# Kernel optimization log

Hardware: AMD Instinct MI355X
Metric: run time of the kernel (lower is better)

The kernel has to match this reference:

```python
import jax, jax.numpy as jnp
import numpy as np
import itertools

DIM = 384
KEY_DIM = 32
NUM_HEADS = 8
ATTN_RATIO = 4
RESOLUTION = 7
D = ATTN_RATIO * KEY_DIM          # 128
DH = D * NUM_HEADS                # 1024
H_QKV = DH + 2 * KEY_DIM * NUM_HEADS  # 1536
B = 2048
N = RESOLUTION ** 2               # 49


def _build_bias_idxs():
    points = list(itertools.product(range(RESOLUTION), range(RESOLUTION)))
    attention_offsets = {}
    idxs = []
    for p1 in points:
        for p2 in points:
            offset = (abs(p1[0] - p2[0]), abs(p1[1] - p2[1]))
            if offset not in attention_offsets:
                attention_offsets[offset] = len(attention_offsets)
            idxs.append(attention_offsets[offset])
    return np.array(idxs, dtype=np.int32).reshape(N, N), len(attention_offsets)


def setup_inputs() -> dict:
    key = jax.random.key(0)
    ks = jax.random.split(key, 6)
    bias_idxs_np, n_offsets = _build_bias_idxs()  # n_offsets == 49 for resolution 7
    x = jax.random.normal(ks[0], (B, N, DIM), dtype=jnp.float32)
    qkv_w = jax.random.normal(ks[1], (H_QKV, DIM), dtype=jnp.float32) * (DIM ** -0.5)
    qkv_b = jnp.zeros((H_QKV,), dtype=jnp.float32)
    proj_w = jax.random.normal(ks[2], (DIM, DH), dtype=jnp.float32) * (DH ** -0.5)
    proj_b = jnp.zeros((DIM,), dtype=jnp.float32)
    attn_bias = jax.random.normal(ks[3], (NUM_HEADS, n_offsets), dtype=jnp.float32) * 0.02
    bias_idxs = jnp.asarray(bias_idxs_np)
    return {"x": x, "qkv_w": qkv_w, "qkv_b": qkv_b, "proj_w": proj_w,
            "proj_b": proj_b, "attn_bias": attn_bias, "bias_idxs": bias_idxs}


def reference(x, qkv_w, qkv_b, proj_w, proj_b, attn_bias, bias_idxs):
    Bb, Nn, _ = x.shape
    scale = KEY_DIM ** -0.5
    qkv = x @ qkv_w.T + qkv_b                       # [B, N, 1536]
    qkv = qkv.reshape(Bb, Nn, NUM_HEADS, KEY_DIM + KEY_DIM + D)
    q = qkv[..., :KEY_DIM]                          # [B, N, H, kd]
    k = qkv[..., KEY_DIM:2 * KEY_DIM]               # [B, N, H, kd]
    v = qkv[..., 2 * KEY_DIM:]                      # [B, N, H, d]
    bias = attn_bias[:, bias_idxs]                  # [H, N, N] gathered rel-pos bias
    attn = jnp.einsum('bnhk,bmhk->bhnm', q, k) * scale + bias
    attn = jax.nn.softmax(attn, axis=-1)
    out = jnp.einsum('bhnm,bmhd->bnhd', attn, v).reshape(Bb, Nn, DH)
    return out @ proj_w.T + proj_b                  # [B, N, dim]
```

## Files before the change

kernel.cpp:

```cpp
#include <hip/hip_runtime.h>
#include <cstddef>
#include <cstdint>

#define TOK    49
#define KD     32
#define NH     8
#define DHEAD  128
#define HQKV   1536
#define DHTOT  1024
#define DIMM   384

typedef unsigned short u16;
typedef float  f32x4  __attribute__((ext_vector_type(4)));
typedef __bf16 bf16x8 __attribute__((ext_vector_type(8)));

typedef const __attribute__((address_space(1))) void gas_void;
typedef __attribute__((address_space(3))) void las_void;

static __device__ __forceinline__ u16 f2bf(float f) {
    unsigned int u = __builtin_bit_cast(unsigned int, f);
    return (u16)((u + 0x7fffu + ((u >> 16) & 1u)) >> 16);
}

static __device__ __forceinline__ int swz(int row, int c) {
    return (row << 6) + ((((c >> 3) ^ (row & 7)) << 3) | (c & 7));
}

static __device__ __forceinline__ int swzV(int row, int c) {
    return (row << 6) + ((((c >> 3) ^ (row & 7) ^ ((row >> 3) & 7)) << 3) | (c & 7));
}

static __device__ __forceinline__ int xcd_chunk(int bid, int nwg) {
    const int xcd = bid & 7, slot = bid >> 3;
    const int q = nwg >> 3, r = nwg & 7;
    return (xcd < r ? xcd * (q + 1) : r * (q + 1) + (xcd - r) * q) + slot;
}

#define BAR() __builtin_amdgcn_s_barrier()
#define WAIT_VM6()  asm volatile("s_waitcnt vmcnt(6)"  ::: "memory")
#define WAIT_VM10() asm volatile("s_waitcnt vmcnt(10)" ::: "memory")
#define WAIT_VM0()  asm volatile("s_waitcnt vmcnt(0)"  ::: "memory")
#define LGKM0_BAR() do { asm volatile("s_waitcnt lgkmcnt(0)" ::: "memory"); \
                         __builtin_amdgcn_s_barrier(); } while (0)

__global__ __launch_bounds__(256)
void cast_swz(const float* __restrict__ in, u16* __restrict__ out, int K8, long nchunk)
{
    long i = (long)blockIdx.x * 256 + threadIdx.x;
    const long stride = (long)gridDim.x * 256;
    for (; i < nchunk; i += stride) {
        const long row = i / K8;
        const int  c8  = (int)(i - row * K8);
        const int  slot = c8 & 7, tpan = c8 >> 3;
        float4 v0 = reinterpret_cast<const float4*>(in)[i * 2];
        float4 v1 = reinterpret_cast<const float4*>(in)[i * 2 + 1];
        uint4 o;
        o.x = f2bf(v0.x) | ((unsigned)f2bf(v0.y) << 16);
        o.y = f2bf(v0.z) | ((unsigned)f2bf(v0.w) << 16);
        o.z = f2bf(v1.x) | ((unsigned)f2bf(v1.y) << 16);
        o.w = f2bf(v1.z) | ((unsigned)f2bf(v1.w) << 16);
        *reinterpret_cast<uint4*>(out + row * (long)K8 * 8 + tpan * 64 +
                                  ((slot ^ ((int)row & 7)) << 3)) = o;
    }
}

__global__ __launch_bounds__(256)
void bias_expand(const float* __restrict__ attn_bias, const int* __restrict__ idxs,
                 float* __restrict__ bias_full, int n_off)
{
    int i = blockIdx.x * 256 + threadIdx.x;
    if (i < NH * TOK * TOK) {
        int h = i / (TOK * TOK), s = i - h * (TOK * TOK);
        bias_full[i] = attn_bias[h * n_off + idxs[s]];
    }
}

static __device__ __forceinline__ int frag_off(int row, int ks8fg) {
    return (row << 6) + (((ks8fg ^ (row & 7)) << 3));
}

__global__ __launch_bounds__(256)
void gemm_qkv(const u16* __restrict__ A,
              const u16* __restrict__ W,
              const float* __restrict__ bias,
              u16* __restrict__ qkvb, int M)
{
    const int K = DIMM;
    const int NB2 = HQKV / 256;
    const int nwg = (M / 64) * NB2;
    const int wgid = xcd_chunk(blockIdx.x, nwg);
    const int bm = (wgid / NB2) * 64;
    const int bn = (wgid % NB2) * 256;

    __shared__ u16 Alds[2][64 * 64];
    __shared__ u16 B0lds[2][128 * 64];
    __shared__ u16 B1lds[2][128 * 64];

    const int t    = threadIdx.x;
    const int lane = t & 63;
    const int wv   = t >> 6;
    const int lrow = lane >> 3;
    const int lcol = (lane & 7) * 8;
    const int frow = lane & 15;
    const int fg   = lane >> 4;

    f32x4 acc0[4][2], acc1[4][2];
    #pragma unroll
    for (int mi = 0; mi < 4; ++mi)
        #pragma unroll
        for (int nc = 0; nc < 2; ++nc) { acc0[mi][nc] = (f32x4)0.0f; acc1[mi][nc] = (f32x4)0.0f; }

    auto STAGE = [&](int buf, int k0) {
        #pragma unroll
        for (int i = 0; i < 2; ++i) {
            const int c   = i * 4 + wv;
            const int row = c * 8 + lrow;
            __builtin_amdgcn_global_load_lds((gas_void*)(A + (size_t)(bm + row) * K + k0 + lcol),
                                             (las_void*)(&Alds[buf][c * 512]), 16, 0, 0);
        }
        #pragma unroll
        for (int i = 0; i < 4; ++i) {
            const int c   = i * 4 + wv;
            const int row = c * 8 + lrow;
            __builtin_amdgcn_global_load_lds((gas_void*)(W + (size_t)(bn + row) * K + k0 + lcol),
                                             (las_void*)(&B0lds[buf][c * 512]), 16, 0, 0);
        }
        #pragma unroll
        for (int i = 0; i < 4; ++i) {
            const int c   = i * 4 + wv;
            const int row = c * 8 + lrow;
            __builtin_amdgcn_global_load_lds((gas_void*)(W + (size_t)(bn + 128 + row) * K + k0 + lcol),
                                             (las_void*)(&B1lds[buf][c * 512]), 16, 0, 0);
        }
    };

    STAGE(0, 0);
    STAGE(1, 64);

    const int NT = 6;
    for (int ts = 0; ts < NT; ++ts) {
        if (ts < NT - 1) { WAIT_VM10(); }
        else             { WAIT_VM0(); }
        BAR();
        const u16* Ab  = Alds[ts & 1];
        const u16* B0b = B0lds[ts & 1];
        const u16* B1b = B1lds[ts & 1];
        #pragma unroll
        for (int ks = 0; ks < 2; ++ks) {
            const int sl = ks * 4 + fg;
            bf16x8 af[4], b0[2], b1[2];
            #pragma unroll
            for (int mi = 0; mi < 4; ++mi)
                af[mi] = *reinterpret_cast<const bf16x8*>(&Ab[frag_off(mi * 16 + frow, sl)]);
            #pragma unroll
            for (int nc = 0; nc < 2; ++nc) {
                b0[nc] = *reinterpret_cast<const bf16x8*>(&B0b[frag_off(wv * 32 + nc * 16 + frow, sl)]);
                b1[nc] = *reinterpret_cast<const bf16x8*>(&B1b[frag_off(wv * 32 + nc * 16 + frow, sl)]);
            }
            #pragma unroll
            for (int mi = 0; mi < 4; ++mi)
                #pragma unroll
                for (int nc = 0; nc < 2; ++nc) {
                    acc0[mi][nc] = __builtin_amdgcn_mfma_f32_16x16x32_bf16(af[mi], b0[nc], acc0[mi][nc], 0, 0, 0);
                    acc1[mi][nc] = __builtin_amdgcn_mfma_f32_16x16x32_bf16(af[mi], b1[nc], acc1[mi][nc], 0, 0, 0);
                }
        }
        BAR();
        if (ts < NT - 2) STAGE(ts & 1, (ts + 2) * 64);
    }

    const int rbase = (lane >> 4) * 4;
    #pragma unroll
    for (int half = 0; half < 2; ++half) {
        #pragma unroll
        for (int nc = 0; nc < 2; ++nc) {
            const int col = bn + half * 128 + wv * 32 + nc * 16 + frow;
            const float bv = bias[col];
            #pragma unroll
            for (int mi = 0; mi < 4; ++mi) {
                #pragma unroll
                for (int j = 0; j < 4; ++j) {
                    const int row = bm + mi * 16 + rbase + j;
                    const float v = half ? acc1[mi][nc][j] : acc0[mi][nc][j];
                    qkvb[(size_t)row * HQKV + col] = f2bf(v + bv);
                }
            }
        }
    }
}

__global__ __launch_bounds__(256)
void gemm_bf16_nt(const u16* __restrict__ A, const u16* __restrict__ W,
                  const float* __restrict__ bias, float* __restrict__ C,
                  int M, int N, int K)
{
    const int NB = N / 128;
    const int nwg = (M / 64) * NB;
    const int wgid = xcd_chunk(blockIdx.x, nwg);
    const int bm = (wgid / NB) * 64;
    const int bn = (wgid % NB) * 128;

    __shared__ u16 Alds[2][64 * 64];
    __shared__ u16 Blds[2][128 * 64];

    const int t    = threadIdx.x;
    const int lane = t & 63;
    const int wv   = t >> 6;
    const int lrow = lane >> 3;
    const int lcol = (lane & 7) * 8;
    const int frow = lane & 15;
    const int fg   = lane >> 4;

    f32x4 acc[4][2];
    #pragma unroll
    for (int mi = 0; mi < 4; ++mi)
        #pragma unroll
        for (int nc = 0; nc < 2; ++nc) acc[mi][nc] = (f32x4)0.0f;

    auto STAGE = [&](int buf, int k0) {
        #pragma unroll
        for (int i = 0; i < 2; ++i) {
            const int c   = i * 4 + wv;
            const int row = c * 8 + lrow;
            __builtin_amdgcn_global_load_lds((gas_void*)(A + (size_t)(bm + row) * K + k0 + lcol),
                                             (las_void*)(&Alds[buf][c * 512]), 16, 0, 0);
        }
        #pragma unroll
        for (int i = 0; i < 4; ++i) {
            const int c   = i * 4 + wv;
            const int row = c * 8 + lrow;
            __builtin_amdgcn_global_load_lds((gas_void*)(W + (size_t)(bn + row) * K + k0 + lcol),
                                             (las_void*)(&Blds[buf][c * 512]), 16, 0, 0);
        }
    };

    const int NT = K / 64;
    STAGE(0, 0);
    STAGE(1, 64);

    for (int ts = 0; ts < NT; ++ts) {
        if (ts < NT - 1) { WAIT_VM6(); }
        else             { WAIT_VM0(); }
        BAR();
        const u16* Ab = Alds[ts & 1];
        const u16* Bb = Blds[ts & 1];
        #pragma unroll
        for (int ks = 0; ks < 2; ++ks) {
            const int sl = ks * 4 + fg;
            bf16x8 af[4], bf[2];
            #pragma unroll
            for (int mi = 0; mi < 4; ++mi)
                af[mi] = *reinterpret_cast<const bf16x8*>(&Ab[frag_off(mi * 16 + frow, sl)]);
            #pragma unroll
            for (int nc = 0; nc < 2; ++nc)
                bf[nc] = *reinterpret_cast<const bf16x8*>(&Bb[frag_off(wv * 32 + nc * 16 + frow, sl)]);
            #pragma unroll
            for (int mi = 0; mi < 4; ++mi)
                #pragma unroll
                for (int nc = 0; nc < 2; ++nc)
                    acc[mi][nc] = __builtin_amdgcn_mfma_f32_16x16x32_bf16(af[mi], bf[nc], acc[mi][nc], 0, 0, 0);
        }
        BAR();
        if (ts < NT - 2) STAGE(ts & 1, (ts + 2) * 64);
    }

    const int rbase = (lane >> 4) * 4;
    #pragma unroll
    for (int nc = 0; nc < 2; ++nc) {
        const int col = bn + wv * 32 + nc * 16 + frow;
        const float bv = bias[col];
        #pragma unroll
        for (int mi = 0; mi < 4; ++mi) {
            #pragma unroll
            for (int j = 0; j < 4; ++j) {
                const int row = bm + mi * 16 + rbase + j;
                C[(size_t)row * N + col] = acc[mi][nc][j] + bv;
            }
        }
    }
}

#define NCH 5
struct Regs { uint4 v[NCH]; };

static __device__ __forceinline__ void load_regs(Regs& r, const u16* __restrict__ base, int t)
{
    #pragma unroll
    for (int k = 0; k < NCH; ++k) {
        const int idx = t + k * 256;
        if (idx < TOK * 24) {
            const int n = idx / 24, c = idx - n * 24;
            r.v[k] = *reinterpret_cast<const uint4*>(base + (size_t)n * HQKV + c * 8);
        }
    }
}

static __device__ __forceinline__ void write_lds(const Regs& r, u16* __restrict__ QK,
                                                 u16* __restrict__ V, int t)
{
    #pragma unroll
    for (int k = 0; k < NCH; ++k) {
        const int idx = t + k * 256;
        if (idx < TOK * 24) {
            const int n = idx / 24, c24 = idx - n * 24;
            if (c24 < 8) {
                *reinterpret_cast<uint4*>(&QK[(n << 6) + ((c24 ^ (n & 7)) << 3)]) = r.v[k];
            } else {
                const int d0 = (c24 - 8) * 8;
                u16 vals[8];
                *reinterpret_cast<uint4*>(vals) = r.v[k];
                #pragma unroll
                for (int e = 0; e < 8; ++e)
                    V[swzV(d0 + e, n)] = vals[e];
            }
        }
    }
}

static __device__ __forceinline__ void attn_head(
    const u16* __restrict__ QK, const u16* __restrict__ V,
    float* __restrict__ S, u16* __restrict__ Ps,
    const float* __restrict__ bh_bias, u16* __restrict__ ab,
    int b, int h, int t)
{
    const int lane = t & 63;
    const int w    = t >> 6;
    const int fr   = lane & 15;
    const int fg   = lane >> 4;

    bf16x8 qf = *reinterpret_cast<const bf16x8*>(&QK[swz(16 * w + fr, fg * 8)]);
    f32x4 sacc[4];
    #pragma unroll
    for (int nj = 0; nj < 4; ++nj) {
        bf16x8 kf = *reinterpret_cast<const bf16x8*>(&QK[swz(16 * nj + fr, 32 + fg * 8)]);
        sacc[nj] = __builtin_amdgcn_mfma_f32_16x16x32_bf16(qf, kf, (f32x4)0.0f, 0, 0, 0);
    }

    const float scale = 0.17677669529663687f;
    #pragma unroll
    for (int nj = 0; nj < 4; ++nj) {
        #pragma unroll
        for (int j = 0; j < 4; ++j) {
            const int row = 16 * w + fg * 4 + j;
            const int col = 16 * nj + fr;
            const int rn = row < TOK ? row : TOK - 1;
            const int cm = col < TOK ? col : TOK - 1;
            S[row * 80 + col] = sacc[nj][j] * scale + bh_bias[rn * TOK + cm];
        }
    }
    LGKM0_BAR();

    {
        const int n = t >> 2, j = t & 3;
        const float* Sr = &S[n * 80];
        float v[16];
        #pragma unroll
        for (int e = 0; e < 8; ++e) v[e]     = Sr[8 * j + e];
        #pragma unroll
        for (int e = 0; e < 8; ++e) v[8 + e] = Sr[32 + 8 * j + e];

        float mx = -1e30f;
        #pragma unroll
        for (int e = 0; e < 8; ++e) mx = fmaxf(mx, v[e]);
        #pragma unroll
        for (int e = 0; e < 8; ++e)
            if (32 + 8 * j + e < TOK) mx = fmaxf(mx, v[8 + e]);
        mx = fmaxf(mx, __shfl_xor(mx, 1, 4));
        mx = fmaxf(mx, __shfl_xor(mx, 2, 4));

        float sum = 0.f;
        #pragma unroll
        for (int e = 0; e < 8; ++e) { v[e] = __expf(v[e] - mx); sum += v[e]; }
        #pragma unroll
        for (int e = 0; e < 8; ++e) {
            const float ev = (32 + 8 * j + e < TOK) ? __expf(v[8 + e] - mx) : 0.f;
            v[8 + e] = ev; sum += ev;
        }
        sum += __shfl_xor(sum, 1, 4);
        sum += __shfl_xor(sum, 2, 4);
        const float inv = 1.f / sum;

        uint4 o;
        o.x = f2bf(v[0] * inv)  | ((unsigned)f2bf(v[1] * inv)  << 16);
        o.y = f2bf(v[2] * inv)  | ((unsigned)f2bf(v[3] * inv)  << 16);
        o.z = f2bf(v[4] * inv)  | ((unsigned)f2bf(v[5] * inv)  << 16);
        o.w = f2bf(v[6] * inv)  | ((unsigned)f2bf(v[7] * inv)  << 16);
        *reinterpret_cast<uint4*>(&Ps[swz(n, 8 * j)]) = o;
        o.x = f2bf(v[8] * inv)  | ((unsigned)f2bf(v[9] * inv)  << 16);
        o.y = f2bf(v[10] * inv) | ((unsigned)f2bf(v[11] * inv) << 16);
        o.z = f2bf(v[12] * inv) | ((unsigned)f2bf(v[13] * inv) << 16);
        o.w = f2bf(v[14] * inv) | ((unsigned)f2bf(v[15] * inv) << 16);
        *reinterpret_cast<uint4*>(&Ps[swz(n, 32 + 8 * j)]) = o;
    }
    LGKM0_BAR();

    f32x4 oacc[8];
    #pragma unroll
    for (int nj = 0; nj < 8; ++nj) oacc[nj] = (f32x4)0.0f;
    #pragma unroll
    for (int ks = 0; ks < 2; ++ks) {
        bf16x8 pf = *reinterpret_cast<const bf16x8*>(&Ps[swz(16 * w + fr, ks * 32 + fg * 8)]);
        #pragma unroll
        for (int nj = 0; nj < 8; ++nj) {
            bf16x8 vf = *reinterpret_cast<const bf16x8*>(&V[swzV(16 * nj + fr, ks * 32 + fg * 8)]);
            oacc[nj] = __builtin_amdgcn_mfma_f32_16x16x32_bf16(pf, vf, oacc[nj], 0, 0, 0);
        }
    }

    #pragma unroll
    for (int nj = 0; nj < 8; ++nj) {
        const int d = 16 * nj + fr;
        const int c = h * DHEAD + d;
        const int tp = c >> 6, sl = (c >> 3) & 7, cc = c & 7;
        #pragma unroll
        for (int j = 0; j < 4; ++j) {
            const int n = 16 * w + fg * 4 + j;
            if (n < TOK) {
                const int gr = b * TOK + n;
                ab[(size_t)gr * DHTOT + (tp << 6) + (((sl ^ (gr & 7)) << 3) | cc)] = f2bf(oacc[nj][j]);
            }
        }
    }
}

__global__ __launch_bounds__(256)
void attn_mfma(const u16* __restrict__ qkvb,
               const float* __restrict__ bias_full,
               u16* __restrict__ ab)
{
    __shared__ __align__(16) u16  QKs[64 * 64];
    __shared__ __align__(16) u16  Vts[128 * 64];
    __shared__ __align__(16) float S[64 * 80];
    __shared__ __align__(16) u16  Ps[64 * 64];

    const int t = threadIdx.x;
    const int b = blockIdx.x;
    const u16* base = qkvb + (size_t)b * TOK * HQKV;

    if (t < 128 * 2) {
        const int row = t >> 1, sl = 6 + (t & 1);
        *reinterpret_cast<uint4*>(&Vts[(row << 6) +
            (((sl ^ (row & 7) ^ ((row >> 3) & 7)) & 7) << 3)]) = make_uint4(0, 0, 0, 0);
    }
    __syncthreads();

    for (int flat = t; flat < TOK * 24; flat += 256) {
        const int n = flat / 24, c24 = flat - n * 24;
        uint4 u = *reinterpret_cast<const uint4*>(base + (size_t)n * HQKV + c24 * 8);
        if (c24 < 8) {
            *reinterpret_cast<uint4*>(&QKs[(n << 6) + ((c24 ^ (n & 7)) << 3)]) = u;
        } else {
            const int d0 = (c24 - 8) * 8;
            u16 vals[8];
            *reinterpret_cast<uint4*>(vals) = u;
            #pragma unroll
            for (int e = 0; e < 8; ++e)
                Vts[swzV(d0 + e, n)] = vals[e];
        }
    }

    Regs r;
    #pragma unroll 1
    for (int i = 0; i < NH; ++i) {
        if (i > 0) write_lds(r, QKs, Vts, t);
        if (i < NH - 1) load_regs(r, base + (i + 1) * 192, t);
        LGKM0_BAR();
        attn_head(QKs, Vts, S, Ps, bias_full + i * (TOK * TOK), ab, b, i, t);
        LGKM0_BAR();
    }
}

extern "C" void kernel_launch(void* const* d_in, const int* in_sizes, int n_in,
                              void* d_out, int out_size, void* d_ws, size_t ws_size,
                              hipStream_t stream)
{
    const float* x         = (const float*)d_in[0];
    const float* qkv_w     = (const float*)d_in[1];
    const float* qkv_b     = (const float*)d_in[2];
    const float* proj_w    = (const float*)d_in[3];
    const float* proj_b    = (const float*)d_in[4];
    const float* attn_bias = (const float*)d_in[5];
    const int*   bias_idxs = (const int*)d_in[6];

    const int Mtot  = in_sizes[0] / DIMM;
    const int Btot  = Mtot / TOK;
    const int n_off = in_sizes[5] / NH;

    const size_t nWq = (size_t)HQKV * DIMM;
    const size_t nWp = (size_t)DIMM * DHTOT;
    float* bias_full = (float*)d_ws;
    u16*   wq        = (u16*)((char*)d_ws + 76832);
    u16*   wp        = wq + nWq;
    u16*   dyn       = wp + nWp;
    const size_t fixed_bytes = 76832 + (nWq + nWp) * sizeof(u16);
    const size_t per_batch = (size_t)TOK * (DIMM + HQKV + DHTOT) * 2;

    if (ws_size <= fixed_bytes) return;
    long BcL = (long)((ws_size - fixed_bytes) / per_batch);
    int Bc = (int)((BcL / 128) * 128);
    if (Bc <= 0) return;
    if (Bc > Btot) Bc = Btot;

    cast_swz<<<dim3(288), 256, 0, stream>>>(qkv_w, wq, DIMM / 8, (long)HQKV * (DIMM / 8));
    cast_swz<<<dim3(192), 256, 0, stream>>>(proj_w, wp, DHTOT / 8, (long)DIMM * (DHTOT / 8));
    bias_expand<<<dim3((NH * TOK * TOK + 255) / 256), 256, 0, stream>>>(attn_bias, bias_idxs, bias_full, n_off);

    for (int b0 = 0; b0 < Btot; b0 += Bc) {
        const int bc = (b0 + Bc <= Btot) ? Bc : (Btot - b0);
        const int Mc = bc * TOK;

        u16* xb   = dyn;
        u16* qkvb = xb   + (size_t)Bc * TOK * DIMM;
        u16* abb  = qkvb + (size_t)Bc * TOK * HQKV;

        const float* xc   = x + (size_t)b0 * TOK * DIMM;
        float*       outc = (float*)d_out + (size_t)b0 * TOK * DIMM;

        cast_swz<<<dim3(2048), 256, 0, stream>>>(xc, xb, DIMM / 8, (long)Mc * (DIMM / 8));

        gemm_qkv<<<dim3((Mc / 64) * (HQKV / 256)), 256, 0, stream>>>(xb, wq, qkv_b, qkvb, Mc);

        attn_mfma<<<dim3(bc), 256, 0, stream>>>(qkvb, bias_full, abb);

        gemm_bf16_nt<<<dim3((Mc / 64) * (DIMM / 128)), 256, 0, stream>>>(abb, wp, proj_b, outc, Mc, DIMM, DHTOT);
    }
}
```

Baseline: 624.2 us.

## Fuse fp32-to-bf16 cast of x into QKV GEMM register-staged A loads

Removes the separate cast_swz pass over x and its bf16 workspace buffer. The QKV GEMM now reads fp32 activations directly into registers, converts them to bf16 and writes them swizzled into LDS, while weights still use direct global-to-LDS loads. This removes one full read and write of x through memory and a kernel launch. In exchange, each A tile is read redundantly by the six N-blocks at double the byte width, and the pipeline gains register pressure and an extra LDS write step before each barrier.

```diff
diff --git a/kernel.cpp b/kernel.cpp
--- a/kernel.cpp
+++ b/kernel.cpp
@@ -38,7 +38,7 @@
 
 #define BAR() __builtin_amdgcn_s_barrier()
 #define WAIT_VM6()  asm volatile("s_waitcnt vmcnt(6)"  ::: "memory")
-#define WAIT_VM10() asm volatile("s_waitcnt vmcnt(10)" ::: "memory")
+#define WAIT_VM12() asm volatile("s_waitcnt vmcnt(12)" ::: "memory")
 #define WAIT_VM0()  asm volatile("s_waitcnt vmcnt(0)"  ::: "memory")
 #define LGKM0_BAR() do { asm volatile("s_waitcnt lgkmcnt(0)" ::: "memory"); \
                          __builtin_amdgcn_s_barrier(); } while (0)
@@ -80,7 +80,7 @@
 }
 
 __global__ __launch_bounds__(256)
-void gemm_qkv(const u16* __restrict__ A,
+void gemm_qkv(const float* __restrict__ X,
               const u16* __restrict__ W,
               const float* __restrict__ bias,
               u16* __restrict__ qkvb, int M)
@@ -104,20 +104,18 @@
     const int frow = lane & 15;
     const int fg   = lane >> 4;
 
+    const int ar0 = t >> 3,           as0 = t & 7;
+    const int ar1 = (t + 256) >> 3,   as1 = t & 7;
+
     f32x4 acc0[4][2], acc1[4][2];
     #pragma unroll
     for (int mi = 0; mi < 4; ++mi)
         #pragma unroll
         for (int nc = 0; nc < 2; ++nc) { acc0[mi][nc] = (f32x4)0.0f; acc1[mi][nc] = (f32x4)0.0f; }
 
-    auto STAGE = [&](int buf, int k0) {
-        #pragma unroll
-        for (int i = 0; i < 2; ++i) {
-            const int c   = i * 4 + wv;
-            const int row = c * 8 + lrow;
-            __builtin_amdgcn_global_load_lds((gas_void*)(A + (size_t)(bm + row) * K + k0 + lcol),
-                                             (las_void*)(&Alds[buf][c * 512]), 16, 0, 0);
-        }
+    uint4 rA[2][4];
+
+    auto ISSUE = [&](int buf, int k0) {
         #pragma unroll
         for (int i = 0; i < 4; ++i) {
             const int c   = i * 4 + wv;
@@ -132,16 +130,38 @@
             __builtin_amdgcn_global_load_lds((gas_void*)(W + (size_t)(bn + 128 + row) * K + k0 + lcol),
                                              (las_void*)(&B1lds[buf][c * 512]), 16, 0, 0);
         }
+        const float* a0 = X + (size_t)(bm + ar0) * K + k0 + as0 * 8;
+        const float* a1 = X + (size_t)(bm + ar1) * K + k0 + as1 * 8;
+        rA[buf][0] = *reinterpret_cast<const uint4*>(a0);
+        rA[buf][1] = *reinterpret_cast<const uint4*>(a0 + 4);
+        rA[buf][2] = *reinterpret_cast<const uint4*>(a1);
+        rA[buf][3] = *reinterpret_cast<const uint4*>(a1 + 4);
     };
 
-    STAGE(0, 0);
-    STAGE(1, 64);
+    auto WRITE = [&](int buf) {
+        #pragma unroll
+        for (int l = 0; l < 2; ++l) {
+            const int row = l ? ar1 : ar0;
+            const int sl  = l ? as1 : as0;
+            const float4 f0 = __builtin_bit_cast(float4, rA[buf][l * 2]);
+            const float4 f1 = __builtin_bit_cast(float4, rA[buf][l * 2 + 1]);
+            uint4 o;
+            o.x = f2bf(f0.x) | ((unsigned)f2bf(f0.y) << 16);
+            o.y = f2bf(f0.z) | ((unsigned)f2bf(f0.w) << 16);
+            o.z = f2bf(f1.x) | ((unsigned)f2bf(f1.y) << 16);
+            o.w = f2bf(f1.z) | ((unsigned)f2bf(f1.w) << 16);
+            *reinterpret_cast<uint4*>(&Alds[buf][(row << 6) + ((sl ^ (row & 7)) << 3)]) = o;
+        }
+    };
+
+    ISSUE(0, 0);
+    ISSUE(1, 64);
 
     const int NT = 6;
     for (int ts = 0; ts < NT; ++ts) {
-        if (ts < NT - 1) { WAIT_VM10(); }
-        else             { WAIT_VM0(); }
-        BAR();
+        WRITE(ts & 1);
+        WAIT_VM12();
+        LGKM0_BAR();
         const u16* Ab  = Alds[ts & 1];
         const u16* B0b = B0lds[ts & 1];
         const u16* B1b = B1lds[ts & 1];
@@ -166,7 +186,7 @@
                 }
         }
         BAR();
-        if (ts < NT - 2) STAGE(ts & 1, (ts + 2) * 64);
+        if (ts < NT - 2) ISSUE(ts & 1, (ts + 2) * 64);
     }
 
     const int rbase = (lane >> 4) * 4;
@@ -493,7 +513,7 @@
     u16*   wp        = wq + nWq;
     u16*   dyn       = wp + nWp;
     const size_t fixed_bytes = 76832 + (nWq + nWp) * sizeof(u16);
-    const size_t per_batch = (size_t)TOK * (DIMM + HQKV + DHTOT) * 2;
+    const size_t per_batch = (size_t)TOK * (HQKV + DHTOT) * 2;
 
     if (ws_size <= fixed_bytes) return;
     long BcL = (long)((ws_size - fixed_bytes) / per_batch);
@@ -509,16 +529,13 @@
         const int bc = (b0 + Bc <= Btot) ? Bc : (Btot - b0);
         const int Mc = bc * TOK;
 
-        u16* xb   = dyn;
-        u16* qkvb = xb   + (size_t)Bc * TOK * DIMM;
+        u16* qkvb = dyn;
         u16* abb  = qkvb + (size_t)Bc * TOK * HQKV;
 
         const float* xc   = x + (size_t)b0 * TOK * DIMM;
         float*       outc = (float*)d_out + (size_t)b0 * TOK * DIMM;
 
-        cast_swz<<<dim3(2048), 256, 0, stream>>>(xc, xb, DIMM / 8, (long)Mc * (DIMM / 8));
-
-        gemm_qkv<<<dim3((Mc / 64) * (HQKV / 256)), 256, 0, stream>>>(xb, wq, qkv_b, qkvb, Mc);
+        gemm_qkv<<<dim3((Mc / 64) * (HQKV / 256)), 256, 0, stream>>>(xc, wq, qkv_b, qkvb, Mc);
 
         attn_mfma<<<dim3(bc), 256, 0, stream>>>(qkvb, bias_full, abb);
 
```

Result: faster. 605.0 us (-3.1%).

## Fuse x cast into QKV GEMM with LDS-resident weight slab and M-chunk streaming

Applied to the files above, without the earlier changes.

The separate fp32→bf16 cast pass over x is removed. The QKV GEMM now reads fp32 x directly from global memory, converting it in registers. Each workgroup keeps a full 64×384 weight slab resident in LDS and streams a 3584-row chunk of M, so weights are reused across many row panels without double buffering. Attention's two LDS barriers are replaced with lgkmcnt waits plus a scheduling fence, which is only safe if each wave reads only what it wrote. The trade-off is uncoalesced, unshared global reads of A, with each wave loading its fragments straight from global memory and no LDS staging.

```diff
diff --git a/kernel.cpp b/kernel.cpp
--- a/kernel.cpp
+++ b/kernel.cpp
@@ -30,6 +30,14 @@
     return (row << 6) + ((((c >> 3) ^ (row & 7) ^ ((row >> 3) & 7)) << 3) | (c & 7));
 }
 
+static __device__ __forceinline__ int frag384(int row, int e) {
+    return row * 384 + (e & ~63) + ((((e >> 3) & 7) ^ (row & 7)) << 3);
+}
+
+static __device__ __forceinline__ int frag_off(int row, int ks8fg) {
+    return (row << 6) + (((ks8fg ^ (row & 7)) << 3));
+}
+
 static __device__ __forceinline__ int xcd_chunk(int bid, int nwg) {
     const int xcd = bid & 7, slot = bid >> 3;
     const int q = nwg >> 3, r = nwg & 7;
@@ -38,10 +46,11 @@
 
 #define BAR() __builtin_amdgcn_s_barrier()
 #define WAIT_VM6()  asm volatile("s_waitcnt vmcnt(6)"  ::: "memory")
-#define WAIT_VM10() asm volatile("s_waitcnt vmcnt(10)" ::: "memory")
 #define WAIT_VM0()  asm volatile("s_waitcnt vmcnt(0)"  ::: "memory")
 #define LGKM0_BAR() do { asm volatile("s_waitcnt lgkmcnt(0)" ::: "memory"); \
                          __builtin_amdgcn_s_barrier(); } while (0)
+#define LGKM0_FENCE() do { asm volatile("s_waitcnt lgkmcnt(0)" ::: "memory"); \
+                           __builtin_amdgcn_sched_barrier(0); } while (0)
 
 __global__ __launch_bounds__(256)
 void cast_swz(const float* __restrict__ in, u16* __restrict__ out, int K8, long nchunk)
@@ -75,117 +84,91 @@
     }
 }
 
-static __device__ __forceinline__ int frag_off(int row, int ks8fg) {
-    return (row << 6) + (((ks8fg ^ (row & 7)) << 3));
-}
-
-__global__ __launch_bounds__(256)
-void gemm_qkv(const u16* __restrict__ A,
+#define MCH 3584
+__global__ __launch_bounds__(256, 3)
+void gemm_qkv(const float* __restrict__ X,
               const u16* __restrict__ W,
               const float* __restrict__ bias,
               u16* __restrict__ qkvb, int M)
 {
-    const int K = DIMM;
-    const int NB2 = HQKV / 256;
-    const int nwg = (M / 64) * NB2;
+    const int nMch = (M + MCH - 1) / MCH;
+    const int nwg  = nMch * 24;
     const int wgid = xcd_chunk(blockIdx.x, nwg);
-    const int bm = (wgid / NB2) * 64;
-    const int bn = (wgid % NB2) * 256;
-
-    __shared__ u16 Alds[2][64 * 64];
-    __shared__ u16 B0lds[2][128 * 64];
-    __shared__ u16 B1lds[2][128 * 64];
+    const int mch  = wgid / 24;
+    const int cb   = wgid % 24;
+    const int bn   = cb * 64;
+
+    __shared__ u16 Wl[64 * 384];
 
     const int t    = threadIdx.x;
     const int lane = t & 63;
-    const int wv   = t >> 6;
-    const int lrow = lane >> 3;
-    const int lcol = (lane & 7) * 8;
-    const int frow = lane & 15;
+    const int w    = t >> 6;
+    const int fr   = lane & 15;
     const int fg   = lane >> 4;
 
-    f32x4 acc0[4][2], acc1[4][2];
-    #pragma unroll
-    for (int mi = 0; mi < 4; ++mi)
-        #pragma unroll
-        for (int nc = 0; nc < 2; ++nc) { acc0[mi][nc] = (f32x4)0.0f; acc1[mi][nc] = (f32x4)0.0f; }
-
-    auto STAGE = [&](int buf, int k0) {
-        #pragma unroll
-        for (int i = 0; i < 2; ++i) {
-            const int c   = i * 4 + wv;
-            const int row = c * 8 + lrow;
-            __builtin_amdgcn_global_load_lds((gas_void*)(A + (size_t)(bm + row) * K + k0 + lcol),
-                                             (las_void*)(&Alds[buf][c * 512]), 16, 0, 0);
-        }
-        #pragma unroll
-        for (int i = 0; i < 4; ++i) {
-            const int c   = i * 4 + wv;
-            const int row = c * 8 + lrow;
-            __builtin_amdgcn_global_load_lds((gas_void*)(W + (size_t)(bn + row) * K + k0 + lcol),
-                                             (las_void*)(&B0lds[buf][c * 512]), 16, 0, 0);
-        }
-        #pragma unroll
-        for (int i = 0; i < 4; ++i) {
-            const int c   = i * 4 + wv;
-            const int row = c * 8 + lrow;
-            __builtin_amdgcn_global_load_lds((gas_void*)(W + (size_t)(bn + 128 + row) * K + k0 + lcol),
-                                             (las_void*)(&B1lds[buf][c * 512]), 16, 0, 0);
-        }
-    };
-
-    STAGE(0, 0);
-    STAGE(1, 64);
-
-    const int NT = 6;
-    for (int ts = 0; ts < NT; ++ts) {
-        if (ts < NT - 1) { WAIT_VM10(); }
-        else             { WAIT_VM0(); }
-        BAR();
-        const u16* Ab  = Alds[ts & 1];
-        const u16* B0b = B0lds[ts & 1];
-        const u16* B1b = B1lds[ts & 1];
-        #pragma unroll
-        for (int ks = 0; ks < 2; ++ks) {
-            const int sl = ks * 4 + fg;
-            bf16x8 af[4], b0[2], b1[2];
-            #pragma unroll
-            for (int mi = 0; mi < 4; ++mi)
-                af[mi] = *reinterpret_cast<const bf16x8*>(&Ab[frag_off(mi * 16 + frow, sl)]);
-            #pragma unroll
-            for (int nc = 0; nc < 2; ++nc) {
-                b0[nc] = *reinterpret_cast<const bf16x8*>(&B0b[frag_off(wv * 32 + nc * 16 + frow, sl)]);
-                b1[nc] = *reinterpret_cast<const bf16x8*>(&B1b[frag_off(wv * 32 + nc * 16 + frow, sl)]);
-            }
-            #pragma unroll
-            for (int mi = 0; mi < 4; ++mi)
+    #pragma unroll
+    for (int i = 0; i < 12; ++i) {
+        const int off = (i * 256 + t) * 8;
+        __builtin_amdgcn_global_load_lds((gas_void*)(W + (size_t)bn * 384 + off),
+                                         (las_void*)(Wl + off), 16, 0, 0);
+    }
+    WAIT_VM0();
+    BAR();
+
+    float bv[4];
+    #pragma unroll
+    for (int nc = 0; nc < 4; ++nc) bv[nc] = bias[bn + nc * 16 + fr];
+
+    const int npan = MCH / 128;
+    for (int p = 0; p < npan; ++p) {
+        const int m0 = mch * MCH + (p * 4 + w) * 32;
+        if (m0 >= M) break;
+
+        f32x4 acc[2][4];
+        #pragma unroll
+        for (int mi = 0; mi < 2; ++mi)
+            #pragma unroll
+            for (int nc = 0; nc < 4; ++nc) acc[mi][nc] = (f32x4)0.0f;
+
+        #pragma unroll
+        for (int half = 0; half < 2; ++half) {
+            bf16x8 a[2][6];
+            #pragma unroll
+            for (int mi = 0; mi < 2; ++mi)
                 #pragma unroll
-                for (int nc = 0; nc < 2; ++nc) {
-                    acc0[mi][nc] = __builtin_amdgcn_mfma_f32_16x16x32_bf16(af[mi], b0[nc], acc0[mi][nc], 0, 0, 0);
-                    acc1[mi][nc] = __builtin_amdgcn_mfma_f32_16x16x32_bf16(af[mi], b1[nc], acc1[mi][nc], 0, 0, 0);
+                for (int q = 0; q < 6; ++q) {
+                    const int kk = half * 6 + q;
+                    const float* ap = X + (size_t)(m0 + mi * 16 + fr) * DIMM + kk * 32 + fg * 8;
+                    const float4 L0 = *reinterpret_cast<const float4*>(ap);
+                    const float4 L1 = *reinterpret_cast<const float4*>(ap + 4);
+                    bf16x8 r;
+                    r[0] = (__bf16)L0.x; r[1] = (__bf16)L0.y;
+                    r[2] = (__bf16)L0.z; r[3] = (__bf16)L0.w;
+                    r[4] = (__bf16)L1.x; r[5] = (__bf16)L1.y;
+                    r[6] = (__bf16)L1.z; r[7] = (__bf16)L1.w;
+                    a[mi][q] = r;
                 }
-        }
-        BAR();
-        if (ts < NT - 2) STAGE(ts & 1, (ts + 2) * 64);
-    }
-
-    const int rbase = (lane >> 4) * 4;
-    #pragma unroll
-    for (int half = 0; half < 2; ++half) {
-        #pragma unroll
-        for (int nc = 0; nc < 2; ++nc) {
-            const int col = bn + half * 128 + wv * 32 + nc * 16 + frow;
-            const float bv = bias[col];
-            #pragma unroll
-            for (int mi = 0; mi < 4; ++mi) {
+            #pragma unroll
+            for (int q = 0; q < 6; ++q) {
+                const int kk = half * 6 + q;
                 #pragma unroll
-                for (int j = 0; j < 4; ++j) {
-                    const int row = bm + mi * 16 + rbase + j;
-                    const float v = half ? acc1[mi][nc][j] : acc0[mi][nc][j];
-                    qkvb[(size_t)row * HQKV + col] = f2bf(v + bv);
+                for (int nc = 0; nc < 4; ++nc) {
+                    bf16x8 bfr = *reinterpret_cast<const bf16x8*>(
+                        &Wl[frag384(nc * 16 + fr, kk * 32 + fg * 8)]);
+                    acc[0][nc] = __builtin_amdgcn_mfma_f32_16x16x32_bf16(a[0][q], bfr, acc[0][nc], 0, 0, 0);
+                    acc[1][nc] = __builtin_amdgcn_mfma_f32_16x16x32_bf16(a[1][q], bfr, acc[1][nc], 0, 0, 0);
                 }
             }
         }
+
+        #pragma unroll
+        for (int mi = 0; mi < 2; ++mi)
+            #pragma unroll
+            for (int nc = 0; nc < 4; ++nc)
+                #pragma unroll
+                for (int j = 0; j < 4; ++j)
+                    qkvb[(size_t)(m0 + mi * 16 + fg * 4 + j) * HQKV + bn + nc * 16 + fr] =
+                        f2bf(acc[mi][nc][j] + bv[nc]);
     }
 }
 
@@ -348,7 +331,7 @@
             S[row * 80 + col] = sacc[nj][j] * scale + bh_bias[rn * TOK + cm];
         }
     }
-    LGKM0_BAR();
+    LGKM0_FENCE();
 
     {
         const int n = t >> 2, j = t & 3;
@@ -392,7 +375,7 @@
         o.w = f2bf(v[14] * inv) | ((unsigned)f2bf(v[15] * inv) << 16);
         *reinterpret_cast<uint4*>(&Ps[swz(n, 32 + 8 * j)]) = o;
     }
-    LGKM0_BAR();
+    LGKM0_FENCE();
 
     f32x4 oacc[8];
     #pragma unroll
@@ -493,7 +476,7 @@
     u16*   wp        = wq + nWq;
     u16*   dyn       = wp + nWp;
     const size_t fixed_bytes = 76832 + (nWq + nWp) * sizeof(u16);
-    const size_t per_batch = (size_t)TOK * (DIMM + HQKV + DHTOT) * 2;
+    const size_t per_batch = (size_t)TOK * (HQKV + DHTOT) * 2;
 
     if (ws_size <= fixed_bytes) return;
     long BcL = (long)((ws_size - fixed_bytes) / per_batch);
@@ -509,16 +492,13 @@
         const int bc = (b0 + Bc <= Btot) ? Bc : (Btot - b0);
         const int Mc = bc * TOK;
 
-        u16* xb   = dyn;
-        u16* qkvb = xb   + (size_t)Bc * TOK * DIMM;
+        u16* qkvb = dyn;
         u16* abb  = qkvb + (size_t)Bc * TOK * HQKV;
 
         const float* xc   = x + (size_t)b0 * TOK * DIMM;
         float*       outc = (float*)d_out + (size_t)b0 * TOK * DIMM;
 
-        cast_swz<<<dim3(2048), 256, 0, stream>>>(xc, xb, DIMM / 8, (long)Mc * (DIMM / 8));
-
-        gemm_qkv<<<dim3((Mc / 64) * (HQKV / 256)), 256, 0, stream>>>(xb, wq, qkv_b, qkvb, Mc);
+        gemm_qkv<<<dim3(((Mc + MCH - 1) / MCH) * 24), 256, 0, stream>>>(xc, wq, qkv_b, qkvb, Mc);
 
         attn_mfma<<<dim3(bc), 256, 0, stream>>>(qkvb, bias_full, abb);
 
```

Result: slower. 851.5 us (+36.4%).
